# Kernel optimization log

Hardware: AMD Instinct MI355X
Metric: run time of the kernel (lower is better)

Reference implementation:

```python
import jax, jax.numpy as jnp
import numpy as np

DIM = 1024
DEPTH = 4
HEADS = 16
MLP = 4096
B, N = 4, 1024
SCALE = DIM ** (-0.5)  # NOTE: module scales by dim^-0.5, not head_dim^-0.5
EPS = 1e-5


def setup_inputs() -> dict:
    key = jax.random.key(0)
    ks = jax.random.split(key, 13)
    s = 0.02
    return {
        "x": jax.random.normal(ks[0], (B, N, DIM), dtype=jnp.float32),
        "ln1_g": jnp.ones((DEPTH, DIM), jnp.float32),
        "ln1_b": jnp.zeros((DEPTH, DIM), jnp.float32),
        "w_qkv": jax.random.normal(ks[1], (DEPTH, DIM, 3 * DIM), jnp.float32) * s,
        "w_out": jax.random.normal(ks[2], (DEPTH, DIM, DIM), jnp.float32) * s,
        "b_out": jnp.zeros((DEPTH, DIM), jnp.float32),
        "ln2_g": jnp.ones((DEPTH, DIM), jnp.float32),
        "ln2_b": jnp.zeros((DEPTH, DIM), jnp.float32),
        "w1": jax.random.normal(ks[3], (DEPTH, DIM, MLP), jnp.float32) * s,
        "b1": jnp.zeros((DEPTH, MLP), jnp.float32),
        "w2": jax.random.normal(ks[4], (DEPTH, MLP, DIM), jnp.float32) * s,
        "b2": jnp.zeros((DEPTH, DIM), jnp.float32),
    }


def _layernorm(x, g, b):
    m = jnp.mean(x, axis=-1, keepdims=True)
    v = jnp.mean(jnp.square(x - m), axis=-1, keepdims=True)
    return (x - m) * jax.lax.rsqrt(v + EPS) * g + b


def _gelu(x):
    # x * 0.5 * (1 + erf(x / sqrt(2)))  (exact GeLu from the module)
    return x * 0.5 * (1.0 + jax.lax.erf(x / jnp.sqrt(2.0).astype(x.dtype)))


def _block(x, p):
    ln1_g, ln1_b, w_qkv, w_out, b_out, ln2_g, ln2_b, w1, b1, w2, b2 = p
    # --- attention (pre-norm, residual) ---
    h = _layernorm(x, ln1_g, ln1_b)
    qkv = h @ w_qkv  # [b, n, 3*dim]
    q, k, v = jnp.split(qkv, 3, axis=-1)
    def heads(t):  # [b, n, dim] -> [b, h, n, d]
        b_, n_, _ = t.shape
        return t.reshape(b_, n_, HEADS, DIM // HEADS).transpose(0, 2, 1, 3)
    q, k, v = heads(q), heads(k), heads(v)
    dots = jnp.einsum('bhid,bhjd->bhij', q, k) * SCALE
    attn = jax.nn.softmax(dots, axis=-1)
    o = jnp.einsum('bhij,bhjd->bhid', attn, v)
    o = o.transpose(0, 2, 1, 3).reshape(x.shape)  # [b, n, dim]
    x = x + (o @ w_out + b_out)
    # --- feed-forward (pre-norm, residual) ---
    h = _layernorm(x, ln2_g, ln2_b)
    x = x + (_gelu(h @ w1 + b1) @ w2 + b2)
    return x


def reference(x, ln1_g, ln1_b, w_qkv, w_out, b_out, ln2_g, ln2_b, w1, b1, w2, b2):
    for l in range(DEPTH):
        p = (ln1_g[l], ln1_b[l], w_qkv[l], w_out[l], b_out[l],
             ln2_g[l], ln2_b[l], w1[l], b1[l], w2[l], b2[l])
        x = _block(x, p)
    return x
```

## Files before the change

kernel.cpp:

```cpp
#include <hip/hip_runtime.h>

typedef __bf16 bf16;
typedef __bf16 bf16x4 __attribute__((ext_vector_type(4)));
typedef __bf16 bf16x8 __attribute__((ext_vector_type(8)));
typedef float  f32x4  __attribute__((ext_vector_type(4)));

#define DIMV   1024
#define MLPV   4096
#define MROWS  4096
#define NHEAD  16
#define SCALEV 0.03125f
#define QKV_LD 3072
#define MB (1024ull * 1024ull)

__device__ __forceinline__ void gload16(const bf16* g, bf16* l) {
    __builtin_amdgcn_global_load_lds((const __attribute__((address_space(1))) unsigned int*)g,
                                     (__attribute__((address_space(3))) unsigned int*)l,
                                     16, 0, 0);
}
__device__ __forceinline__ void sb0()        { __builtin_amdgcn_sched_barrier(0); }
__device__ __forceinline__ void wait_vm6()   { asm volatile("s_waitcnt vmcnt(6)" ::: "memory"); }
__device__ __forceinline__ void wait_vm0()   { asm volatile("s_waitcnt vmcnt(0)" ::: "memory"); }
__device__ __forceinline__ void wait_lgkm0() { asm volatile("s_waitcnt lgkmcnt(0)" ::: "memory"); }

__global__ __launch_bounds__(256) void k_ln(const float* __restrict__ x,
                                            const float* __restrict__ g,
                                            const float* __restrict__ b,
                                            bf16* __restrict__ h) {
    int row = blockIdx.x;
    int tid = threadIdx.x;
    const f32x4 v = ((const f32x4*)(x + (size_t)row * DIMV))[tid];
    float s  = v[0]+v[1]+v[2]+v[3];
    float sq = v[0]*v[0]+v[1]*v[1]+v[2]*v[2]+v[3]*v[3];
    for (int m = 1; m < 64; m <<= 1) { s += __shfl_xor(s, m, 64); sq += __shfl_xor(sq, m, 64); }
    __shared__ float ss[4], ssq[4];
    int w = tid >> 6, lane = tid & 63;
    if (lane == 0) { ss[w] = s; ssq[w] = sq; }
    __syncthreads();
    s  = ss[0]+ss[1]+ss[2]+ss[3];
    sq = ssq[0]+ssq[1]+ssq[2]+ssq[3];
    float mean = s * (1.f/DIMV);
    float var  = sq * (1.f/DIMV) - mean*mean;
    float rs   = rsqrtf(var + 1e-5f);
    int c0 = tid * 4;
    const f32x4 gv = ((const f32x4*)(g))[tid];
    const f32x4 bv = ((const f32x4*)(b))[tid];
    bf16x4 o;
    for (int i = 0; i < 4; i++)
        o[i] = (bf16)((v[i]-mean)*rs*gv[i] + bv[i]);
    *(bf16x4*)(h + (size_t)row * DIMV + c0) = o;
}

__global__ __launch_bounds__(256) void k_transpose_cvt(const float* __restrict__ in,
                                                       bf16* __restrict__ out, int R, int C) {
    __shared__ float tile[32][33];
    int tx = threadIdx.x & 31, ty = threadIdx.x >> 5;
    int r0 = blockIdx.y * 32, c0 = blockIdx.x * 32;
    for (int i = 0; i < 4; i++)
        tile[ty + 8*i][tx] = in[(size_t)(r0 + ty + 8*i) * C + c0 + tx];
    __syncthreads();
    for (int i = 0; i < 4; i++)
        out[(size_t)(c0 + ty + 8*i) * R + r0 + tx] = (bf16)tile[tx][ty + 8*i];
}

__global__ __launch_bounds__(256) void k_vt(const bf16* __restrict__ big, bf16* __restrict__ vT) {
    __shared__ bf16 tile[32][33];
    int tx = threadIdx.x & 31, ty = threadIdx.x >> 5;
    int hd0 = blockIdx.x * 32, s0 = blockIdx.y * 32, bb = blockIdx.z;
    const bf16* src = big + (size_t)bb * 1024 * QKV_LD + 2048;
    for (int i = 0; i < 4; i++)
        tile[ty + 8*i][tx] = src[(size_t)(s0 + ty + 8*i) * QKV_LD + hd0 + tx];
    __syncthreads();
    bf16* dst = vT + (size_t)bb * 1024 * 1024;
    for (int i = 0; i < 4; i++)
        dst[(size_t)(hd0 + ty + 8*i) * 1024 + s0 + tx] = tile[tx][ty + 8*i];
}

template<int EPI>
__global__ __launch_bounds__(256) void k_gemm(const bf16* __restrict__ A,
                                              const bf16* __restrict__ Bt,
                                              const float* __restrict__ bias,
                                              bf16* __restrict__ Cb,
                                              float* __restrict__ Cacc,
                                              int N, int K) {
    __shared__ alignas(16) bf16 As[3][128 * 64];
    __shared__ alignas(16) bf16 Bs[3][64 * 64];
    const int tid  = threadIdx.x;
    const int lane = tid & 63, w = tid >> 6;
    const int quad = lane >> 4, l16 = lane & 15;

    const int gx   = (int)gridDim.x;
    const int nwg  = gx * (int)gridDim.y;
    const int orig = (int)blockIdx.y * gx + (int)blockIdx.x;
    const int qq = nwg >> 3, rr = nwg & 7;
    const int xcd = orig & 7, loc = orig >> 3;
    const int wg  = (xcd < rr ? xcd * (qq + 1) : rr * (qq + 1) + (xcd - rr) * qq) + loc;
    const int bn = wg % gx, bm = wg / gx;

    const bf16* Ag = A  + (size_t)bm * 128 * K;
    const bf16* Bg = Bt + (size_t)bn * 64 * K;

    const int srow = lane >> 3;
    const int scol = lane & 7;
    const int sswz = (scol ^ srow) << 3;

    f32x4 acc[2][4];
    f32x4 zero = {0.f,0.f,0.f,0.f};
    for (int mt = 0; mt < 2; mt++) for (int nt = 0; nt < 4; nt++) acc[mt][nt] = zero;

    auto stage = [&](int p, int t) {
        int k0 = t << 6;
        #pragma unroll
        for (int i = 0; i < 4; i++) {
            int row = w * 32 + i * 8;
            gload16(&Ag[(size_t)(row + srow) * K + k0 + sswz], &As[p][row * 64]);
        }
        #pragma unroll
        for (int i = 0; i < 2; i++) {
            int row = w * 16 + i * 8;
            gload16(&Bg[(size_t)(row + srow) * K + k0 + sswz], &Bs[p][row * 64]);
        }
    };

    const int NT = K >> 6;
    stage(0, 0);
    stage(1, 1);
    wait_vm6();
    sb0(); __builtin_amdgcn_s_barrier(); sb0();

    for (int t = 0; t < NT; t++) {
        const int p = t % 3;
        const bool more = (t + 2 < NT);
        if (more) stage((t + 2) % 3, t + 2);
        sb0();

        bf16x8 af[2][2], bfr[4][2];
        #pragma unroll
        for (int mt = 0; mt < 2; mt++)
            #pragma unroll
            for (int ks = 0; ks < 2; ks++) {
                int row = w * 32 + mt * 16 + l16;
                int kb  = ks * 4 + quad;
                af[mt][ks] = *(const bf16x8*)&As[p][row * 64 + ((kb ^ (row & 7)) << 3)];
            }
        #pragma unroll
        for (int nt = 0; nt < 4; nt++)
            #pragma unroll
            for (int ks = 0; ks < 2; ks++) {
                int row = nt * 16 + l16;
                int kb  = ks * 4 + quad;
                bfr[nt][ks] = *(const bf16x8*)&Bs[p][row * 64 + ((kb ^ (row & 7)) << 3)];
            }
        __builtin_amdgcn_s_setprio(1);
        #pragma unroll
        for (int ks = 0; ks < 2; ks++)
            #pragma unroll
            for (int mt = 0; mt < 2; mt++)
                #pragma unroll
                for (int nt = 0; nt < 4; nt++)
                    acc[mt][nt] = __builtin_amdgcn_mfma_f32_16x16x32_bf16(af[mt][ks], bfr[nt][ks], acc[mt][nt], 0, 0, 0);
        __builtin_amdgcn_s_setprio(0);

        sb0();
        wait_lgkm0();
        if (more) wait_vm6();
        else      wait_vm0();
        sb0(); __builtin_amdgcn_s_barrier(); sb0();
    }

    for (int mt = 0; mt < 2; mt++) for (int nt = 0; nt < 4; nt++) {
        int col = bn * 64 + nt * 16 + l16;
        float bval = (EPI >= 1) ? bias[col] : 0.f;
        for (int r = 0; r < 4; r++) {
            int row = bm * 128 + w * 32 + mt * 16 + quad * 4 + r;
            float v = acc[mt][nt][r];
            if (EPI == 0) {
                Cb[(size_t)row * N + col] = (bf16)v;
            } else if (EPI == 1) {
                float t = v + bval;
                float ge = 0.5f * t * (1.f + erff(t * 0.70710678118f));
                Cb[(size_t)row * N + col] = (bf16)ge;
            } else {
                Cacc[(size_t)row * N + col] += v + bval;
            }
        }
    }
}

__global__ __launch_bounds__(256) void k_attn(const bf16* __restrict__ qkv,
                                              const bf16* __restrict__ vT,
                                              bf16* __restrict__ o) {
    const int qt = blockIdx.x;
    const int h  = blockIdx.y;
    const int bb = blockIdx.z;
    const int tid  = threadIdx.x;
    const int lane = tid & 63, w = tid >> 6;
    const int quad = lane >> 4, l16 = lane & 15;
    const int srow = lane >> 3, scol = lane & 7;
    const int sswz = (scol ^ srow) << 3;

    __shared__ alignas(16) bf16 Qs[128 * 64];
    __shared__ alignas(16) bf16 Ks[2][64 * 64];
    __shared__ alignas(16) bf16 Vs[2][64 * 64];
    __shared__ alignas(16) bf16 Ps[128 * 72];

    const bf16* qbase  = qkv + (size_t)(bb*1024 + qt*128) * QKV_LD + h*64;
    const bf16* kbase0 = qkv + (size_t)(bb*1024) * QKV_LD + 1024 + h*64;
    const bf16* vbase0 = vT  + ((size_t)bb*1024 + h*64) * 1024;

    #pragma unroll
    for (int i = 0; i < 4; i++) {
        int row = w * 32 + i * 8;
        gload16(&qbase[(size_t)(row + srow) * QKV_LD + sswz], &Qs[row * 64]);
    }
    auto stageKV = [&](int p, int kt) {
        #pragma unroll
        for (int i = 0; i < 2; i++) {
            int row = w * 16 + i * 8;
            gload16(&kbase0[(size_t)(kt*64 + row + srow) * QKV_LD + sswz], &Ks[p][row * 64]);
            gload16(&vbase0[(size_t)(row + srow) * 1024 + kt*64 + sswz],   &Vs[p][row * 64]);
        }
    };

    f32x4 o_acc[2][4];
    f32x4 zero = {0.f,0.f,0.f,0.f};
    for (int mt = 0; mt < 2; mt++) for (int nt = 0; nt < 4; nt++) o_acc[mt][nt] = zero;
    float l_st[2][4];
    for (int mt = 0; mt < 2; mt++) for (int r = 0; r < 4; r++) l_st[mt][r] = 0.f;

    stageKV(0, 0);
    __syncthreads();

    for (int kt = 0; kt < 16; kt++) {
        const int p = kt & 1;
        if (kt < 15) stageKV(p ^ 1, kt + 1);

        f32x4 sv[2][4];
        __builtin_amdgcn_s_setprio(1);
        for (int mt = 0; mt < 2; mt++) for (int nt = 0; nt < 4; nt++) {
            f32x4 a = zero;
            #pragma unroll
            for (int ks = 0; ks < 2; ks++) {
                int kb = ks * 4 + quad;
                bf16x8 qf = *(const bf16x8*)&Qs[(w*32 + mt*16 + l16) * 64 + ((kb ^ (l16 & 7)) << 3)];
                bf16x8 kf = *(const bf16x8*)&Ks[p][(nt*16 + l16) * 64 + ((kb ^ (l16 & 7)) << 3)];
                a = __builtin_amdgcn_mfma_f32_16x16x32_bf16(qf, kf, a, 0, 0, 0);
            }
            sv[mt][nt] = a;
        }
        __builtin_amdgcn_s_setprio(0);

        for (int mt = 0; mt < 2; mt++) for (int r = 0; r < 4; r++) {
            float rs = 0.f;
            for (int nt = 0; nt < 4; nt++) {
                float pe = __expf(sv[mt][nt][r] * SCALEV);
                sv[mt][nt][r] = pe;
                rs += pe;
            }
            for (int msk = 1; msk < 16; msk <<= 1) rs += __shfl_xor(rs, msk, 64);
            l_st[mt][r] += rs;
        }

        for (int mt = 0; mt < 2; mt++) for (int nt = 0; nt < 4; nt++)
            for (int r = 0; r < 4; r++)
                Ps[(w*32 + mt*16 + quad*4 + r) * 72 + nt*16 + l16] = (bf16)sv[mt][nt][r];
        asm volatile("s_waitcnt lgkmcnt(0)" ::: "memory");
        __builtin_amdgcn_sched_barrier(0);

        __builtin_amdgcn_s_setprio(1);
        for (int mt = 0; mt < 2; mt++) for (int nt = 0; nt < 4; nt++) {
            f32x4 a = o_acc[mt][nt];
            #pragma unroll
            for (int ks = 0; ks < 2; ks++) {
                int kb = ks * 4 + quad;
                bf16x8 pf = *(const bf16x8*)&Ps[(w*32 + mt*16 + l16) * 72 + ks*32 + quad*8];
                bf16x8 vf = *(const bf16x8*)&Vs[p][(nt*16 + l16) * 64 + ((kb ^ (l16 & 7)) << 3)];
                a = __builtin_amdgcn_mfma_f32_16x16x32_bf16(pf, vf, a, 0, 0, 0);
            }
            o_acc[mt][nt] = a;
        }
        __builtin_amdgcn_s_setprio(0);

        __syncthreads();
    }

    for (int mt = 0; mt < 2; mt++) for (int nt = 0; nt < 4; nt++)
        for (int r = 0; r < 4; r++) {
            float val = o_acc[mt][nt][r] / l_st[mt][r];
            int row = qt*128 + w*32 + mt*16 + quad*4 + r;
            o[(size_t)(bb*1024 + row) * DIMV + h*64 + nt*16 + l16] = (bf16)val;
        }
}

extern "C" void kernel_launch(void* const* d_in, const int* in_sizes, int n_in,
                              void* d_out, int out_size, void* d_ws, size_t ws_size,
                              hipStream_t stream) {
    (void)in_sizes; (void)n_in; (void)out_size;
    const float* x_in  = (const float*)d_in[0];
    const float* ln1_g = (const float*)d_in[1];
    const float* ln1_b = (const float*)d_in[2];
    const float* w_qkv = (const float*)d_in[3];
    const float* w_out = (const float*)d_in[4];
    const float* b_out = (const float*)d_in[5];
    const float* ln2_g = (const float*)d_in[6];
    const float* ln2_b = (const float*)d_in[7];
    const float* w1    = (const float*)d_in[8];
    const float* b1    = (const float*)d_in[9];
    const float* w2    = (const float*)d_in[10];
    const float* b2    = (const float*)d_in[11];

    char* ws = (char*)d_ws;
    float* xf32    = (float*)ws;
    bf16*  h       = (bf16*)(ws + 16*MB);
    bf16*  wT1     = (bf16*)(ws + 24*MB);
    bf16*  wT2     = (bf16*)(ws + 32*MB);
    bf16*  attn_o  = (bf16*)(ws + 40*MB);
    bf16*  big     = (bf16*)(ws + 48*MB);
    size_t bigsz   = (ws_size > 48*MB) ? (ws_size - 48*MB) : 0;

    int G = 4;
    while (G > 1 && (size_t)G * 8*MB > bigsz) G >>= 1;
    int RC = 4096;
    while (RC > 128 && (size_t)RC * 8192ull > bigsz) RC >>= 1;

    bf16* vT = big + (size_t)G * 1024 * QKV_LD;

    hipMemcpyAsync(xf32, x_in, (size_t)MROWS * DIMV * sizeof(float),
                   hipMemcpyDeviceToDevice, stream);

    for (int l = 0; l < 4; l++) {
        k_ln<<<MROWS, 256, 0, stream>>>(xf32, ln1_g + (size_t)l*DIMV, ln1_b + (size_t)l*DIMV, h);
        k_transpose_cvt<<<dim3(3072/32, 1024/32), 256, 0, stream>>>(w_qkv + (size_t)l*DIMV*3072, wT1, 1024, 3072);
        for (int g = 0; g < 4; g += G) {
            k_gemm<0><<<dim3(3072/64, (G*1024)/128), 256, 0, stream>>>(
                h + (size_t)g*1024*DIMV, wT1, (const float*)nullptr, big, (float*)nullptr, 3072, 1024);
            k_vt<<<dim3(32, 32, G), 256, 0, stream>>>(big, vT);
            k_attn<<<dim3(8, NHEAD, G), 256, 0, stream>>>(big, vT, attn_o + (size_t)g*1024*DIMV);
        }
        k_transpose_cvt<<<dim3(1024/32, 1024/32), 256, 0, stream>>>(w_out + (size_t)l*DIMV*DIMV, wT1, 1024, 1024);
        k_gemm<2><<<dim3(1024/64, 4096/128), 256, 0, stream>>>(
            attn_o, wT1, b_out + (size_t)l*DIMV, (bf16*)nullptr, xf32, 1024, 1024);

        k_ln<<<MROWS, 256, 0, stream>>>(xf32, ln2_g + (size_t)l*DIMV, ln2_b + (size_t)l*DIMV, h);
        k_transpose_cvt<<<dim3(4096/32, 1024/32), 256, 0, stream>>>(w1 + (size_t)l*DIMV*MLPV, wT1, 1024, 4096);
        k_transpose_cvt<<<dim3(1024/32, 4096/32), 256, 0, stream>>>(w2 + (size_t)l*MLPV*DIMV, wT2, 4096, 1024);
        for (int r0 = 0; r0 < 4096; r0 += RC) {
            k_gemm<1><<<dim3(4096/64, RC/128), 256, 0, stream>>>(
                h + (size_t)r0*DIMV, wT1, b1 + (size_t)l*MLPV, big, (float*)nullptr, 4096, 1024);
            k_gemm<2><<<dim3(1024/64, RC/128), 256, 0, stream>>>(
                big, wT2, b2 + (size_t)l*DIMV, (bf16*)nullptr, xf32 + (size_t)r0*DIMV, 1024, 4096);
        }
    }

    hipMemcpyAsync(d_out, xf32, (size_t)MROWS * DIMV * sizeof(float),
                   hipMemcpyDeviceToDevice, stream);
}
```

Baseline: 1.388 ms.

## Use 128x128 GEMM tiles with double buffering for QKV, out-proj and FFN1

Templates the GEMM on output-tile width and switches the QKV, attention-output and FFN1 GEMMs to 128x128 tiles with a 2x2 wave layout and 4x4 MFMA accumulators per wave. Each loaded A and B element is reused across more MFMAs, cutting global and LDS traffic per FLOP. The pipeline for these GEMMs changes from a three-stage buffer with fine-grained waitcnts and setprio to a simpler two-stage buffer with __syncthreads. The FFN2 GEMM keeps the old 128x64 three-stage kernel as a separate copy. The trade-offs are fewer workgroups per GEMM, higher register pressure, and possibly less latency hiding from the simpler pipeline.

```diff
diff --git a/kernel.cpp b/kernel.cpp
--- a/kernel.cpp
+++ b/kernel.cpp
@@ -76,18 +76,21 @@
         dst[(size_t)(hd0 + ty + 8*i) * 1024 + s0 + tx] = tile[tx][ty + 8*i];
 }
 
-template<int EPI>
+template<int EPI, int TN>
 __global__ __launch_bounds__(256) void k_gemm(const bf16* __restrict__ A,
                                               const bf16* __restrict__ Bt,
                                               const float* __restrict__ bias,
                                               bf16* __restrict__ Cb,
                                               float* __restrict__ Cacc,
                                               int N, int K) {
-    __shared__ alignas(16) bf16 As[3][128 * 64];
-    __shared__ alignas(16) bf16 Bs[3][64 * 64];
+    constexpr int NWN = TN / 64;
+    constexpr int MT  = (TN == 128) ? 4 : 2;
+    __shared__ alignas(16) bf16 As[2][128 * 64];
+    __shared__ alignas(16) bf16 Bs[2][TN * 64];
     const int tid  = threadIdx.x;
     const int lane = tid & 63, w = tid >> 6;
     const int quad = lane >> 4, l16 = lane & 15;
+    const int wm = w / NWN, wn = w % NWN;
 
     const int gx   = (int)gridDim.x;
     const int nwg  = gx * (int)gridDim.y;
@@ -98,48 +101,43 @@
     const int bn = wg % gx, bm = wg / gx;
 
     const bf16* Ag = A  + (size_t)bm * 128 * K;
-    const bf16* Bg = Bt + (size_t)bn * 64 * K;
+    const bf16* Bg = Bt + (size_t)bn * TN * K;
 
     const int srow = lane >> 3;
     const int scol = lane & 7;
     const int sswz = (scol ^ srow) << 3;
 
-    f32x4 acc[2][4];
+    f32x4 acc[MT][4];
     f32x4 zero = {0.f,0.f,0.f,0.f};
-    for (int mt = 0; mt < 2; mt++) for (int nt = 0; nt < 4; nt++) acc[mt][nt] = zero;
-
-    auto stage = [&](int p, int t) {
-        int k0 = t << 6;
+    for (int mt = 0; mt < MT; mt++) for (int nt = 0; nt < 4; nt++) acc[mt][nt] = zero;
+
+    auto stage = [&](int p, int k0) {
         #pragma unroll
         for (int i = 0; i < 4; i++) {
             int row = w * 32 + i * 8;
             gload16(&Ag[(size_t)(row + srow) * K + k0 + sswz], &As[p][row * 64]);
         }
         #pragma unroll
-        for (int i = 0; i < 2; i++) {
-            int row = w * 16 + i * 8;
+        for (int i = 0; i < TN / 32; i++) {
+            int row = w * (TN / 4) + i * 8;
             gload16(&Bg[(size_t)(row + srow) * K + k0 + sswz], &Bs[p][row * 64]);
         }
     };
 
     const int NT = K >> 6;
     stage(0, 0);
-    stage(1, 1);
-    wait_vm6();
-    sb0(); __builtin_amdgcn_s_barrier(); sb0();
+    __syncthreads();
 
     for (int t = 0; t < NT; t++) {
-        const int p = t % 3;
-        const bool more = (t + 2 < NT);
-        if (more) stage((t + 2) % 3, t + 2);
-        sb0();
-
-        bf16x8 af[2][2], bfr[4][2];
-        #pragma unroll
-        for (int mt = 0; mt < 2; mt++)
-            #pragma unroll
-            for (int ks = 0; ks < 2; ks++) {
-                int row = w * 32 + mt * 16 + l16;
+        const int p = t & 1;
+        if (t + 1 < NT) stage(p ^ 1, (t + 1) << 6);
+
+        bf16x8 af[MT][2], bfr[4][2];
+        #pragma unroll
+        for (int mt = 0; mt < MT; mt++)
+            #pragma unroll
+            for (int ks = 0; ks < 2; ks++) {
+                int row = wm * (MT * 16) + mt * 16 + l16;
                 int kb  = ks * 4 + quad;
                 af[mt][ks] = *(const bf16x8*)&As[p][row * 64 + ((kb ^ (row & 7)) << 3)];
             }
@@ -147,32 +145,26 @@
         for (int nt = 0; nt < 4; nt++)
             #pragma unroll
             for (int ks = 0; ks < 2; ks++) {
-                int row = nt * 16 + l16;
+                int row = wn * 64 + nt * 16 + l16;
                 int kb  = ks * 4 + quad;
                 bfr[nt][ks] = *(const bf16x8*)&Bs[p][row * 64 + ((kb ^ (row & 7)) << 3)];
             }
-        __builtin_amdgcn_s_setprio(1);
         #pragma unroll
         for (int ks = 0; ks < 2; ks++)
             #pragma unroll
-            for (int mt = 0; mt < 2; mt++)
+            for (int mt = 0; mt < MT; mt++)
                 #pragma unroll
                 for (int nt = 0; nt < 4; nt++)
                     acc[mt][nt] = __builtin_amdgcn_mfma_f32_16x16x32_bf16(af[mt][ks], bfr[nt][ks], acc[mt][nt], 0, 0, 0);
-        __builtin_amdgcn_s_setprio(0);
-
-        sb0();
-        wait_lgkm0();
-        if (more) wait_vm6();
-        else      wait_vm0();
-        sb0(); __builtin_amdgcn_s_barrier(); sb0();
-    }
-
-    for (int mt = 0; mt < 2; mt++) for (int nt = 0; nt < 4; nt++) {
-        int col = bn * 64 + nt * 16 + l16;
+
+        __syncthreads();
+    }
+
+    for (int mt = 0; mt < MT; mt++) for (int nt = 0; nt < 4; nt++) {
+        int col = bn * TN + wn * 64 + nt * 16 + l16;
         float bval = (EPI >= 1) ? bias[col] : 0.f;
         for (int r = 0; r < 4; r++) {
-            int row = bm * 128 + w * 32 + mt * 16 + quad * 4 + r;
+            int row = bm * 128 + wm * (MT * 16) + mt * 16 + quad * 4 + r;
             float v = acc[mt][nt][r];
             if (EPI == 0) {
                 Cb[(size_t)row * N + col] = (bf16)v;
@@ -183,6 +175,106 @@
             } else {
                 Cacc[(size_t)row * N + col] += v + bval;
             }
+        }
+    }
+}
+
+__global__ __launch_bounds__(256) void k_gemm3(const bf16* __restrict__ A,
+                                               const bf16* __restrict__ Bt,
+                                               const float* __restrict__ bias,
+                                               float* __restrict__ Cacc,
+                                               int N, int K) {
+    __shared__ alignas(16) bf16 As[3][128 * 64];
+    __shared__ alignas(16) bf16 Bs[3][64 * 64];
+    const int tid  = threadIdx.x;
+    const int lane = tid & 63, w = tid >> 6;
+    const int quad = lane >> 4, l16 = lane & 15;
+
+    const int gx   = (int)gridDim.x;
+    const int nwg  = gx * (int)gridDim.y;
+    const int orig = (int)blockIdx.y * gx + (int)blockIdx.x;
+    const int qq = nwg >> 3, rr = nwg & 7;
+    const int xcd = orig & 7, loc = orig >> 3;
+    const int wg  = (xcd < rr ? xcd * (qq + 1) : rr * (qq + 1) + (xcd - rr) * qq) + loc;
+    const int bn = wg % gx, bm = wg / gx;
+
+    const bf16* Ag = A  + (size_t)bm * 128 * K;
+    const bf16* Bg = Bt + (size_t)bn * 64 * K;
+
+    const int srow = lane >> 3;
+    const int scol = lane & 7;
+    const int sswz = (scol ^ srow) << 3;
+
+    f32x4 acc[2][4];
+    f32x4 zero = {0.f,0.f,0.f,0.f};
+    for (int mt = 0; mt < 2; mt++) for (int nt = 0; nt < 4; nt++) acc[mt][nt] = zero;
+
+    auto stage = [&](int p, int t) {
+        int k0 = t << 6;
+        #pragma unroll
+        for (int i = 0; i < 4; i++) {
+            int row = w * 32 + i * 8;
+            gload16(&Ag[(size_t)(row + srow) * K + k0 + sswz], &As[p][row * 64]);
+        }
+        #pragma unroll
+        for (int i = 0; i < 2; i++) {
+            int row = w * 16 + i * 8;
+            gload16(&Bg[(size_t)(row + srow) * K + k0 + sswz], &Bs[p][row * 64]);
+        }
+    };
+
+    const int NT = K >> 6;
+    stage(0, 0);
+    stage(1, 1);
+    wait_vm6();
+    sb0(); __builtin_amdgcn_s_barrier(); sb0();
+
+    for (int t = 0; t < NT; t++) {
+        const int p = t % 3;
+        const bool more = (t + 2 < NT);
+        if (more) stage((t + 2) % 3, t + 2);
+        sb0();
+
+        bf16x8 af[2][2], bfr[4][2];
+        #pragma unroll
+        for (int mt = 0; mt < 2; mt++)
+            #pragma unroll
+            for (int ks = 0; ks < 2; ks++) {
+                int row = w * 32 + mt * 16 + l16;
+                int kb  = ks * 4 + quad;
+                af[mt][ks] = *(const bf16x8*)&As[p][row * 64 + ((kb ^ (row & 7)) << 3)];
+            }
+        #pragma unroll
+        for (int nt = 0; nt < 4; nt++)
+            #pragma unroll
+            for (int ks = 0; ks < 2; ks++) {
+                int row = nt * 16 + l16;
+                int kb  = ks * 4 + quad;
+                bfr[nt][ks] = *(const bf16x8*)&Bs[p][row * 64 + ((kb ^ (row & 7)) << 3)];
+            }
+        __builtin_amdgcn_s_setprio(1);
+        #pragma unroll
+        for (int ks = 0; ks < 2; ks++)
+            #pragma unroll
+            for (int mt = 0; mt < 2; mt++)
+                #pragma unroll
+                for (int nt = 0; nt < 4; nt++)
+                    acc[mt][nt] = __builtin_amdgcn_mfma_f32_16x16x32_bf16(af[mt][ks], bfr[nt][ks], acc[mt][nt], 0, 0, 0);
+        __builtin_amdgcn_s_setprio(0);
+
+        sb0();
+        wait_lgkm0();
+        if (more) wait_vm6();
+        else      wait_vm0();
+        sb0(); __builtin_amdgcn_s_barrier(); sb0();
+    }
+
+    for (int mt = 0; mt < 2; mt++) for (int nt = 0; nt < 4; nt++) {
+        int col = bn * 64 + nt * 16 + l16;
+        float bval = bias[col];
+        for (int r = 0; r < 4; r++) {
+            int row = bm * 128 + w * 32 + mt * 16 + quad * 4 + r;
+            Cacc[(size_t)row * N + col] += acc[mt][nt][r] + bval;
         }
     }
 }
@@ -332,23 +424,23 @@
         k_ln<<<MROWS, 256, 0, stream>>>(xf32, ln1_g + (size_t)l*DIMV, ln1_b + (size_t)l*DIMV, h);
         k_transpose_cvt<<<dim3(3072/32, 1024/32), 256, 0, stream>>>(w_qkv + (size_t)l*DIMV*3072, wT1, 1024, 3072);
         for (int g = 0; g < 4; g += G) {
-            k_gemm<0><<<dim3(3072/64, (G*1024)/128), 256, 0, stream>>>(
+            k_gemm<0,128><<<dim3(3072/128, (G*1024)/128), 256, 0, stream>>>(
                 h + (size_t)g*1024*DIMV, wT1, (const float*)nullptr, big, (float*)nullptr, 3072, 1024);
             k_vt<<<dim3(32, 32, G), 256, 0, stream>>>(big, vT);
             k_attn<<<dim3(8, NHEAD, G), 256, 0, stream>>>(big, vT, attn_o + (size_t)g*1024*DIMV);
         }
         k_transpose_cvt<<<dim3(1024/32, 1024/32), 256, 0, stream>>>(w_out + (size_t)l*DIMV*DIMV, wT1, 1024, 1024);
-        k_gemm<2><<<dim3(1024/64, 4096/128), 256, 0, stream>>>(
+        k_gemm<2,128><<<dim3(1024/128, 4096/128), 256, 0, stream>>>(
             attn_o, wT1, b_out + (size_t)l*DIMV, (bf16*)nullptr, xf32, 1024, 1024);
 
         k_ln<<<MROWS, 256, 0, stream>>>(xf32, ln2_g + (size_t)l*DIMV, ln2_b + (size_t)l*DIMV, h);
         k_transpose_cvt<<<dim3(4096/32, 1024/32), 256, 0, stream>>>(w1 + (size_t)l*DIMV*MLPV, wT1, 1024, 4096);
         k_transpose_cvt<<<dim3(1024/32, 4096/32), 256, 0, stream>>>(w2 + (size_t)l*MLPV*DIMV, wT2, 4096, 1024);
         for (int r0 = 0; r0 < 4096; r0 += RC) {
-            k_gemm<1><<<dim3(4096/64, RC/128), 256, 0, stream>>>(
+            k_gemm<1,128><<<dim3(4096/128, RC/128), 256, 0, stream>>>(
                 h + (size_t)r0*DIMV, wT1, b1 + (size_t)l*MLPV, big, (float*)nullptr, 4096, 1024);
-            k_gemm<2><<<dim3(1024/64, RC/128), 256, 0, stream>>>(
-                big, wT2, b2 + (size_t)l*DIMV, (bf16*)nullptr, xf32 + (size_t)r0*DIMV, 1024, 4096);
+            k_gemm3<<<dim3(1024/64, RC/128), 256, 0, stream>>>(
+                big, wT2, b2 + (size_t)l*DIMV, xf32 + (size_t)r0*DIMV, 1024, 4096);
         }
     }
 
```

Result: faster. 1.292 ms (-6.9%).
